# Kernel tuning notes

Hardware: AMD Instinct MI355X
Metric: run time of the kernel (lower is better)

Reference implementation:

```python
import jax, jax.numpy as jnp
import numpy as np

N = 8192
H = 512
E = 262144
NUM_LAYERS = 2
LAYER_DECAY = 0.4
INIT_W = 1e-05


def setup_inputs() -> dict:
    key = jax.random.key(0)
    ks = jax.random.split(key, 6)
    x = jax.random.normal(ks[0], (N, H), dtype=jnp.float32)
    rows = jax.random.randint(ks[1], (E,), 0, N, dtype=jnp.int32)
    cols = jax.random.randint(ks[2], (E,), 0, N, dtype=jnp.int32)
    vals = jax.random.uniform(ks[3], (E,), dtype=jnp.float32)
    # near-identity init as in GSS_GNNLayer (torch Linear: y = x @ W.T + b)
    W1 = jax.random.normal(ks[4], (H, H), dtype=jnp.float32) * INIT_W + jnp.eye(H, dtype=jnp.float32)
    b1 = jnp.zeros((H,), dtype=jnp.float32)
    W2 = jax.random.normal(ks[5], (H, H), dtype=jnp.float32) * INIT_W + jnp.eye(H, dtype=jnp.float32)
    b2 = jnp.zeros((H,), dtype=jnp.float32)
    return {"x": x, "rows": rows, "cols": cols, "vals": vals,
            "W1": W1, "b1": b1, "W2": W2, "b2": b2}


def _spmm(rows, cols, vals, dense):
    # sparse [N,N] @ dense [N,H] via gather + segment-sum scatter-add
    return jax.ops.segment_sum(vals[:, None] * dense[cols], rows, num_segments=N)


def _gcn_layer(x, rows, cols, vals, W1, b1, W2, b2):
    Ax = _spmm(rows, cols, vals, x)                      # [N,H]
    pre1 = Ax @ W1.T + b1
    Ax_x = _spmm(rows, cols, vals, Ax * x)               # A(Ax * x)
    pre2 = Ax_x @ W2.T + b2
    pre = pre1 + pre2
    return pre, jax.nn.elu(pre)


def reference(x, rows, cols, vals, W1, b1, W2, b2):
    residual = None
    for _ in range(NUM_LAYERS):  # shared weights across layers, as in source
        pre, x = _gcn_layer(x, rows, cols, vals, W1, b1, W2, b2)
        if residual is not None:
            x = residual + LAYER_DECAY * x
        residual = pre
    # decoder: row-wise L2 normalize (eps=1e-12 like F.normalize), dense gram, relu
    norm = jnp.maximum(jnp.linalg.norm(x, axis=1, keepdims=True), 1e-12)
    hidden_emb = x / norm
    adj_preds = jax.nn.relu(hidden_emb @ hidden_emb.T)   # [N,N]
    return adj_preds, hidden_emb
```

## Files before the change

### kernel.cpp

```cpp
#include <hip/hip_runtime.h>

#define N_NODES 8192
#define HDIM    512
#define NEDGE   262144

typedef __attribute__((ext_vector_type(8))) short bf16x8;
typedef __attribute__((ext_vector_type(4))) short bf16x4;
typedef __attribute__((ext_vector_type(4))) float f32x4;

__device__ inline unsigned short f2bf(float f) {
  unsigned u = __float_as_uint(f);
  unsigned r = (u + 0x7FFFu + ((u >> 16) & 1u)) >> 16;
  return (unsigned short)r;
}
__device__ inline float bf2f(short s) {
  return __uint_as_float(((unsigned)(unsigned short)s) << 16);
}

__device__ inline void gload16(const void* g, void* l) {
  __builtin_amdgcn_global_load_lds(
      (const __attribute__((address_space(1))) unsigned*)g,
      (__attribute__((address_space(3))) unsigned*)l, 16, 0, 0);
}

__global__ void hist_kernel(const int* __restrict__ rows, int* __restrict__ counts) {
  int e = blockIdx.x * 256 + threadIdx.x;
  atomicAdd(&counts[rows[e]], 1);
}

__global__ __launch_bounds__(1024) void scan_kernel(const int* __restrict__ counts,
                                                    int* __restrict__ offs,
                                                    int* __restrict__ cursor) {
  __shared__ int s[1024];
  int tid = threadIdx.x;
  int local[8];
  int sum = 0;
#pragma unroll
  for (int i = 0; i < 8; ++i) { local[i] = counts[tid * 8 + i]; sum += local[i]; }
  s[tid] = sum;
  __syncthreads();
  for (int d = 1; d < 1024; d <<= 1) {
    int v = (tid >= d) ? s[tid - d] : 0;
    __syncthreads();
    s[tid] += v;
    __syncthreads();
  }
  int base = (tid > 0) ? s[tid - 1] : 0;
#pragma unroll
  for (int i = 0; i < 8; ++i) {
    offs[tid * 8 + i] = base;
    cursor[tid * 8 + i] = base;
    base += local[i];
  }
  if (tid == 1023) offs[8192] = base;
}

__global__ void scatter_kernel(const int* __restrict__ rows, const int* __restrict__ cols,
                               const float* __restrict__ vals, int* cursor,
                               int2* __restrict__ edges) {
  int e = blockIdx.x * 256 + threadIdx.x;
  int slot = atomicAdd(&cursor[rows[e]], 1);
  edges[slot] = make_int2(cols[e], __float_as_int(vals[e]));
}

template <int MODE>
__global__ __launch_bounds__(256) void spmm_bf(const int* __restrict__ offs,
                                               const int2* __restrict__ edges,
                                               const short* __restrict__ Xbf,
                                               const float* __restrict__ aux,
                                               short* __restrict__ outb,
                                               short* __restrict__ prodb) {
  int row = blockIdx.x * 4 + (threadIdx.x >> 6);
  int lane = threadIdx.x & 63;
  int h0 = lane * 8;
  float acc[8] = {0.f, 0.f, 0.f, 0.f, 0.f, 0.f, 0.f, 0.f};
  int e0 = offs[row], e1 = offs[row + 1];
  int p = e0;

  int2 ma0, ma1, ma2, ma3;
  bf16x8 xa0, xa1, xa2, xa3;

  if (p + 4 <= e1) {
    ma0 = edges[p]; ma1 = edges[p + 1]; ma2 = edges[p + 2]; ma3 = edges[p + 3];
    xa0 = *reinterpret_cast<const bf16x8*>(Xbf + (size_t)ma0.x * HDIM + h0);
    xa1 = *reinterpret_cast<const bf16x8*>(Xbf + (size_t)ma1.x * HDIM + h0);
    xa2 = *reinterpret_cast<const bf16x8*>(Xbf + (size_t)ma2.x * HDIM + h0);
    xa3 = *reinterpret_cast<const bf16x8*>(Xbf + (size_t)ma3.x * HDIM + h0);
    p += 4;
    for (; p + 4 <= e1; p += 4) {
      int2 mb0 = edges[p], mb1 = edges[p + 1], mb2 = edges[p + 2], mb3 = edges[p + 3];
      bf16x8 xb0 = *reinterpret_cast<const bf16x8*>(Xbf + (size_t)mb0.x * HDIM + h0);
      bf16x8 xb1 = *reinterpret_cast<const bf16x8*>(Xbf + (size_t)mb1.x * HDIM + h0);
      bf16x8 xb2 = *reinterpret_cast<const bf16x8*>(Xbf + (size_t)mb2.x * HDIM + h0);
      bf16x8 xb3 = *reinterpret_cast<const bf16x8*>(Xbf + (size_t)mb3.x * HDIM + h0);
      float v0 = __int_as_float(ma0.y), v1 = __int_as_float(ma1.y);
      float v2 = __int_as_float(ma2.y), v3 = __int_as_float(ma3.y);
#pragma unroll
      for (int j = 0; j < 8; ++j) {
        acc[j] = fmaf(v0, bf2f(xa0[j]), acc[j]);
        acc[j] = fmaf(v1, bf2f(xa1[j]), acc[j]);
        acc[j] = fmaf(v2, bf2f(xa2[j]), acc[j]);
        acc[j] = fmaf(v3, bf2f(xa3[j]), acc[j]);
      }
      ma0 = mb0; ma1 = mb1; ma2 = mb2; ma3 = mb3;
      xa0 = xb0; xa1 = xb1; xa2 = xb2; xa3 = xb3;
    }
    {
      float v0 = __int_as_float(ma0.y), v1 = __int_as_float(ma1.y);
      float v2 = __int_as_float(ma2.y), v3 = __int_as_float(ma3.y);
#pragma unroll
      for (int j = 0; j < 8; ++j) {
        acc[j] = fmaf(v0, bf2f(xa0[j]), acc[j]);
        acc[j] = fmaf(v1, bf2f(xa1[j]), acc[j]);
        acc[j] = fmaf(v2, bf2f(xa2[j]), acc[j]);
        acc[j] = fmaf(v3, bf2f(xa3[j]), acc[j]);
      }
    }
  }
  for (; p < e1; ++p) {
    int2 e = edges[p];
    float v = __int_as_float(e.y);
    bf16x8 xr = *reinterpret_cast<const bf16x8*>(Xbf + (size_t)e.x * HDIM + h0);
#pragma unroll
    for (int j = 0; j < 8; ++j) acc[j] = fmaf(v, bf2f(xr[j]), acc[j]);
  }

  bf16x8 o;
#pragma unroll
  for (int j = 0; j < 8; ++j) o[j] = (short)f2bf(acc[j]);
  *reinterpret_cast<bf16x8*>(outb + (size_t)row * 1024 + h0) = o;
  if (MODE != 2) {
    const float4* ap = reinterpret_cast<const float4*>(aux + (size_t)row * HDIM + h0);
    float4 a0 = ap[0], a1 = ap[1];
    float xv[8] = {a0.x, a0.y, a0.z, a0.w, a1.x, a1.y, a1.z, a1.w};
    if (MODE == 1) {
#pragma unroll
      for (int j = 0; j < 8; ++j) xv[j] = xv[j] > 0.f ? xv[j] : expm1f(xv[j]);
    }
    bf16x8 t;
#pragma unroll
    for (int j = 0; j < 8; ++j) t[j] = (short)f2bf(acc[j] * xv[j]);
    *reinterpret_cast<bf16x8*>(prodb + (size_t)row * HDIM + h0) = t;
  }
}

__device__ inline void cast8(const float* src, short* dst) {
  const float4* p = reinterpret_cast<const float4*>(src);
  float4 a = p[0], b = p[1];
  bf16x8 o;
  o[0] = (short)f2bf(a.x); o[1] = (short)f2bf(a.y);
  o[2] = (short)f2bf(a.z); o[3] = (short)f2bf(a.w);
  o[4] = (short)f2bf(b.x); o[5] = (short)f2bf(b.y);
  o[6] = (short)f2bf(b.z); o[7] = (short)f2bf(b.w);
  *reinterpret_cast<bf16x8*>(dst) = o;
}

__global__ void prep_kernel(const float* __restrict__ x,
                            const float* __restrict__ W1, const float* __restrict__ W2,
                            const float* __restrict__ b1, const float* __restrict__ b2,
                            short* __restrict__ Xbf, short* __restrict__ Bbuf,
                            float* __restrict__ b12) {
  int b = blockIdx.x;
  if (b < 2048) {
    int t = b * 256 + threadIdx.x;
    int row = t >> 6, c0 = (t & 63) * 8;
    cast8(x + (size_t)row * 512 + c0, Xbf + (size_t)row * 512 + c0);
  } else if (b < 2176) {
    int t = (b - 2048) * 256 + threadIdx.x;
    int row = t >> 6, c0 = (t & 63) * 8;
    cast8(W1 + (size_t)row * 512 + c0, Bbuf + (size_t)row * 1024 + c0);
  } else if (b < 2304) {
    int t = (b - 2176) * 256 + threadIdx.x;
    int row = t >> 6, c0 = (t & 63) * 8;
    cast8(W2 + (size_t)row * 512 + c0, Bbuf + (size_t)row * 1024 + 512 + c0);
  } else {
    int j = threadIdx.x;
    b12[j] = b1[j] + b2[j];
    b12[j + 256] = b1[j + 256] + b2[j + 256];
  }
}

__global__ __launch_bounds__(256) void rownorm_kernel(const float* __restrict__ X,
                                                      float* __restrict__ outf,
                                                      short* __restrict__ outb) {
  int row = blockIdx.x * 4 + (threadIdx.x >> 6);
  int lane = threadIdx.x & 63;
  int h0 = lane * 8;
  const float4* p = reinterpret_cast<const float4*>(X + (size_t)row * HDIM + h0);
  float4 a = p[0], b = p[1];
  float s = a.x * a.x + a.y * a.y + a.z * a.z + a.w * a.w +
            b.x * b.x + b.y * b.y + b.z * b.z + b.w * b.w;
#pragma unroll
  for (int off = 1; off < 64; off <<= 1) s += __shfl_xor(s, off, 64);
  float inv = 1.f / fmaxf(sqrtf(s), 1e-12f);
  a.x *= inv; a.y *= inv; a.z *= inv; a.w *= inv;
  b.x *= inv; b.y *= inv; b.z *= inv; b.w *= inv;
  float4* q = reinterpret_cast<float4*>(outf + (size_t)row * HDIM + h0);
  q[0] = a; q[1] = b;
  bf16x8 o;
  o[0] = (short)f2bf(a.x); o[1] = (short)f2bf(a.y);
  o[2] = (short)f2bf(a.z); o[3] = (short)f2bf(a.w);
  o[4] = (short)f2bf(b.x); o[5] = (short)f2bf(b.y);
  o[6] = (short)f2bf(b.z); o[7] = (short)f2bf(b.w);
  *reinterpret_cast<bf16x8*>(outb + (size_t)row * HDIM + h0) = o;
}

template <int MODE>
__global__ __launch_bounds__(256) void gemm_lds(const short* __restrict__ A,
                                                const short* __restrict__ B,
                                                int N, int K, int nbn,
                                                const float* __restrict__ bias,
                                                const float* __restrict__ resid,
                                                float* __restrict__ out0,
                                                short* __restrict__ out1bf) {
  __shared__ __align__(16) short la[128 * 64];
  __shared__ __align__(16) short lb[128 * 64];

  int q = gridDim.x >> 3;
  int id = (blockIdx.x & 7) * q + (blockIdx.x >> 3);
  int bn = (id % nbn) * 128;
  int bm = (id / nbn) * 128;

  int lane = threadIdx.x & 63;
  int wave = threadIdx.x >> 6;

  int rsub = lane >> 3;
  int csrc = (lane & 7) ^ rsub;
  size_t ldkB = (size_t)K * 2;
  const char* gA0 = (const char*)A + (size_t)(bm + wave * 32 + rsub) * ldkB + csrc * 16;
  const char* gB0 = (const char*)B + (size_t)(bn + wave * 32 + rsub) * ldkB + csrc * 16;
  char* lA0 = (char*)la + wave * 4096;
  char* lB0 = (char*)lb + wave * 4096;

  f32x4 zero = {0.f, 0.f, 0.f, 0.f};
  f32x4 acc[4][4];
#pragma unroll
  for (int m = 0; m < 4; ++m)
#pragma unroll
    for (int n = 0; n < 4; ++n) acc[m][n] = zero;

  int rlo = lane & 15;
  int khi = lane >> 4;
  int wm = wave >> 1, wn = wave & 1;

  for (int k0 = 0; k0 < K; k0 += 64) {
    __syncthreads();
#pragma unroll
    for (int j = 0; j < 4; ++j) {
      gload16(gA0 + (size_t)j * 8 * ldkB + (size_t)k0 * 2, lA0 + j * 1024);
      gload16(gB0 + (size_t)j * 8 * ldkB + (size_t)k0 * 2, lB0 + j * 1024);
    }
    __syncthreads();
#pragma unroll
    for (int kk = 0; kk < 2; ++kk) {
      bf16x8 av[4], bv[4];
#pragma unroll
      for (int m = 0; m < 4; ++m) {
        int ra = wm * 64 + m * 16 + rlo;
        int pc = (kk * 4 + khi) ^ (ra & 7);
        av[m] = *reinterpret_cast<const bf16x8*>((const char*)la + ra * 128 + pc * 16);
      }
#pragma unroll
      for (int n = 0; n < 4; ++n) {
        int rb = wn * 64 + n * 16 + rlo;
        int pc = (kk * 4 + khi) ^ (rb & 7);
        bv[n] = *reinterpret_cast<const bf16x8*>((const char*)lb + rb * 128 + pc * 16);
      }
#pragma unroll
      for (int m = 0; m < 4; ++m)
#pragma unroll
        for (int n = 0; n < 4; ++n)
          acc[m][n] = __builtin_amdgcn_mfma_f32_16x16x32_bf16(av[m], bv[n], acc[m][n], 0, 0, 0);
    }
  }

  int obm = bm + wm * 64;
  int obn = bn + wn * 64;
  int crow = (lane >> 4) * 4;
  int ccol = lane & 15;
#pragma unroll
  for (int n = 0; n < 4; ++n) {
    int c = obn + n * 16 + ccol;
    float bc = bias[c];
#pragma unroll
    for (int m = 0; m < 4; ++m) {
#pragma unroll
      for (int v = 0; v < 4; ++v) {
        int r = obm + m * 16 + crow + v;
        size_t idx = (size_t)r * N + c;
        float val = acc[m][n][v];
        if (MODE == 0) {
          float pvl = val + bc;
          out0[idx] = pvl;
          float e = pvl > 0.f ? pvl : expm1f(pvl);
          out1bf[idx] = (short)f2bf(e);
        } else {
          float pvl = val + bc;
          out0[idx] = resid[idx] + 0.4f * (pvl > 0.f ? pvl : expm1f(pvl));
        }
      }
    }
  }
}

__global__ __launch_bounds__(512, 4) void gram256(const short* __restrict__ H,
                                                  float* __restrict__ out) {
  __shared__ __align__(16) char lds[3 * 24576];
  const int NK = HDIM / 32;

  int id = (blockIdx.x & 7) * 256 + (blockIdx.x >> 3);
  int st = id >> 4, wt = id & 15;
  int bm = ((st >> 3) * 4 + (wt >> 2)) * 128;
  int bn = ((st & 7) * 4 + (wt & 3)) * 256;

  int tid = threadIdx.x;
  int wid = tid >> 6;
  int lane = tid & 63;
  int wr = wid >> 2;
  int wc = wid & 3;
  int rlo = lane & 15;
  int khi = lane >> 4;
  int wbase = wid * 1024;

  const char* Ab = (const char*)H + (size_t)bm * 1024;
  const char* Bb = (const char*)H + (size_t)bn * 1024;
  int r4 = tid >> 2, c4 = tid & 3;

  f32x4 zero = {0.f, 0.f, 0.f, 0.f};
  f32x4 acc[4][4];
#pragma unroll
  for (int m = 0; m < 4; ++m)
#pragma unroll
    for (int n = 0; n < 4; ++n) acc[m][n] = zero;

  auto stage = [&](int s) {
    char* slot = lds + (s % 3) * 24576;
    size_t go = (size_t)s * 64 + c4 * 16;
    gload16(Ab + (size_t)r4 * 1024 + go,         slot + wbase);
    gload16(Bb + (size_t)r4 * 1024 + go,         slot + 8192 + wbase);
    gload16(Bb + (size_t)(r4 + 128) * 1024 + go, slot + 16384 + wbase);
  };

  stage(0);

  for (int s = 0; s < NK; ++s) {
    if (s + 1 < NK) {
      stage(s + 1);
      asm volatile("s_waitcnt vmcnt(3)" ::: "memory");
    } else {
      asm volatile("s_waitcnt vmcnt(0)" ::: "memory");
    }
    __builtin_amdgcn_s_barrier();
    __builtin_amdgcn_sched_barrier(0);

    const char* slot = lds + (s % 3) * 24576;
    bf16x8 av[4], bv[4];
#pragma unroll
    for (int m = 0; m < 4; ++m)
      av[m] = *reinterpret_cast<const bf16x8*>(
          slot + (wr * 64 + m * 16 + rlo) * 64 + khi * 16);
#pragma unroll
    for (int n = 0; n < 4; ++n)
      bv[n] = *reinterpret_cast<const bf16x8*>(
          slot + 8192 + (wc * 64 + n * 16 + rlo) * 64 + khi * 16);

    __builtin_amdgcn_s_setprio(1);
#pragma unroll
    for (int m = 0; m < 4; ++m)
#pragma unroll
      for (int n = 0; n < 4; ++n)
        acc[m][n] = __builtin_amdgcn_mfma_f32_16x16x32_bf16(av[m], bv[n], acc[m][n], 0, 0, 0);
    __builtin_amdgcn_s_setprio(0);
  }

  int obm = bm + wr * 64;
  int obn = bn + wc * 64;
  int crow = khi * 4;
#pragma unroll
  for (int m = 0; m < 4; ++m) {
#pragma unroll
    for (int n = 0; n < 4; ++n) {
      int c = obn + n * 16 + rlo;
#pragma unroll
      for (int v = 0; v < 4; ++v) {
        int r = obm + m * 16 + crow + v;
        float val = acc[m][n][v];
        out[(size_t)r * N_NODES + c] = val > 0.f ? val : 0.f;
      }
    }
  }
}

extern "C" void kernel_launch(void* const* d_in, const int* in_sizes, int n_in,
                              void* d_out, int out_size, void* d_ws, size_t ws_size,
                              hipStream_t stream) {
  const float* x  = (const float*)d_in[0];
  const int* rows = (const int*)d_in[1];
  const int* cols = (const int*)d_in[2];
  const float* vals = (const float*)d_in[3];
  const float* W1 = (const float*)d_in[4];
  const float* b1 = (const float*)d_in[5];
  const float* W2 = (const float*)d_in[6];
  const float* b2 = (const float*)d_in[7];

  float* out_adj = (float*)d_out;
  float* out_hid = out_adj + (size_t)N_NODES * N_NODES;

  char* w = (char*)d_ws;
  size_t off = 0;
  auto alloc = [&](size_t bytes) -> void* {
    void* p = w + off;
    off += (bytes + 255) & ~(size_t)255;
    return p;
  };
  int* counts   = (int*)alloc(8192 * sizeof(int));
  int* offs     = (int*)alloc(8193 * sizeof(int));
  int* cursor   = (int*)alloc(8192 * sizeof(int));
  int2* edges   = (int2*)alloc((size_t)NEDGE * sizeof(int2));
  float* b12    = (float*)alloc(HDIM * sizeof(float));
  short* Xbf    = (short*)alloc((size_t)N_NODES * HDIM * sizeof(short));
  short* Tbf    = (short*)alloc((size_t)N_NODES * HDIM * sizeof(short));
  short* Abuf   = (short*)alloc((size_t)N_NODES * 1024 * sizeof(short));
  short* Bbuf   = (short*)alloc((size_t)512 * 1024 * sizeof(short));
  float* pre1   = (float*)alloc((size_t)N_NODES * HDIM * sizeof(float));
  float* Hf     = (float*)alloc((size_t)N_NODES * HDIM * sizeof(float));
  short* Hbuf   = (short*)alloc((size_t)N_NODES * HDIM * sizeof(short));

  hipMemsetAsync(counts, 0, 8192 * sizeof(int), stream);
  hist_kernel<<<NEDGE / 256, 256, 0, stream>>>(rows, counts);
  scan_kernel<<<1, 1024, 0, stream>>>(counts, offs, cursor);
  scatter_kernel<<<NEDGE / 256, 256, 0, stream>>>(rows, cols, vals, cursor, edges);

  prep_kernel<<<2305, 256, 0, stream>>>(x, W1, W2, b1, b2, Xbf, Bbuf, b12);

  spmm_bf<0><<<2048, 256, 0, stream>>>(offs, edges, Xbf, x, Abuf, Tbf);
  spmm_bf<2><<<2048, 256, 0, stream>>>(offs, edges, Tbf, nullptr, Abuf + 512, nullptr);
  gemm_lds<0><<<256, 256, 0, stream>>>(Abuf, Bbuf, 512, 1024, 4, b12, nullptr, pre1, Xbf);

  spmm_bf<1><<<2048, 256, 0, stream>>>(offs, edges, Xbf, pre1, Abuf, Tbf);
  spmm_bf<2><<<2048, 256, 0, stream>>>(offs, edges, Tbf, nullptr, Abuf + 512, nullptr);
  gemm_lds<1><<<256, 256, 0, stream>>>(Abuf, Bbuf, 512, 1024, 4, b12, pre1, Hf, nullptr);

  rownorm_kernel<<<2048, 256, 0, stream>>>(Hf, out_hid, Hbuf);
  gram256<<<2048, 512, 0, stream>>>(Hbuf, out_adj);
}
```

Baseline: 327.3 us.

## Add triple-buffered async LDS ring to dense GEMM, fuse histogram into prep

Replaces the GEMM's synchronous load-then-compute K loop (two barriers per 64-wide step) with a three-slot LDS ring. Two K=32 stages are prefetched ahead, paced by vmcnt waits and a single barrier per step. The gram kernel's prefetch moves from one stage ahead to two, with the next load issued after the barrier. The edge histogram is folded into the prep kernel to remove one launch. These changes aim to hide global-load latency and cut launch overhead, at the cost of dropping the XOR-swizzled LDS layout, which may bring bank conflicts.

After: 315.7 us. 1.04x faster.

```diff
diff --git a/kernel.cpp b/kernel.cpp
--- a/kernel.cpp
+++ b/kernel.cpp
@@ -5,7 +5,6 @@
 #define NEDGE   262144
 
 typedef __attribute__((ext_vector_type(8))) short bf16x8;
-typedef __attribute__((ext_vector_type(4))) short bf16x4;
 typedef __attribute__((ext_vector_type(4))) float f32x4;
 
 __device__ inline unsigned short f2bf(float f) {
@@ -23,9 +22,11 @@
       (__attribute__((address_space(3))) unsigned*)l, 16, 0, 0);
 }
 
-__global__ void hist_kernel(const int* __restrict__ rows, int* __restrict__ counts) {
-  int e = blockIdx.x * 256 + threadIdx.x;
-  atomicAdd(&counts[rows[e]], 1);
+__device__ inline void wait_vmcnt_c(int n) {
+  if (n == 8)      asm volatile("s_waitcnt vmcnt(8)" ::: "memory");
+  else if (n == 4) asm volatile("s_waitcnt vmcnt(4)" ::: "memory");
+  else if (n == 3) asm volatile("s_waitcnt vmcnt(3)" ::: "memory");
+  else             asm volatile("s_waitcnt vmcnt(0)" ::: "memory");
 }
 
 __global__ __launch_bounds__(1024) void scan_kernel(const int* __restrict__ counts,
@@ -155,22 +156,26 @@
   *reinterpret_cast<bf16x8*>(dst) = o;
 }
 
-__global__ void prep_kernel(const float* __restrict__ x,
+__global__ void prep_kernel(const int* __restrict__ rows, int* __restrict__ counts,
+                            const float* __restrict__ x,
                             const float* __restrict__ W1, const float* __restrict__ W2,
                             const float* __restrict__ b1, const float* __restrict__ b2,
                             short* __restrict__ Xbf, short* __restrict__ Bbuf,
                             float* __restrict__ b12) {
   int b = blockIdx.x;
-  if (b < 2048) {
-    int t = b * 256 + threadIdx.x;
+  if (b < 1024) {
+    int e = b * 256 + threadIdx.x;
+    atomicAdd(&counts[rows[e]], 1);
+  } else if (b < 3072) {
+    int t = (b - 1024) * 256 + threadIdx.x;
     int row = t >> 6, c0 = (t & 63) * 8;
     cast8(x + (size_t)row * 512 + c0, Xbf + (size_t)row * 512 + c0);
-  } else if (b < 2176) {
-    int t = (b - 2048) * 256 + threadIdx.x;
+  } else if (b < 3200) {
+    int t = (b - 3072) * 256 + threadIdx.x;
     int row = t >> 6, c0 = (t & 63) * 8;
     cast8(W1 + (size_t)row * 512 + c0, Bbuf + (size_t)row * 1024 + c0);
-  } else if (b < 2304) {
-    int t = (b - 2176) * 256 + threadIdx.x;
+  } else if (b < 3328) {
+    int t = (b - 3200) * 256 + threadIdx.x;
     int row = t >> 6, c0 = (t & 63) * 8;
     cast8(W2 + (size_t)row * 512 + c0, Bbuf + (size_t)row * 1024 + 512 + c0);
   } else {
@@ -206,31 +211,33 @@
 }
 
 template <int MODE>
-__global__ __launch_bounds__(256) void gemm_lds(const short* __restrict__ A,
-                                                const short* __restrict__ B,
-                                                int N, int K, int nbn,
-                                                const float* __restrict__ bias,
-                                                const float* __restrict__ resid,
-                                                float* __restrict__ out0,
-                                                short* __restrict__ out1bf) {
-  __shared__ __align__(16) short la[128 * 64];
-  __shared__ __align__(16) short lb[128 * 64];
+__global__ __launch_bounds__(256) void gemm_ring(const short* __restrict__ A,
+                                                 const short* __restrict__ B,
+                                                 int N, int K, int nbn,
+                                                 const float* __restrict__ bias,
+                                                 const float* __restrict__ resid,
+                                                 float* __restrict__ out0,
+                                                 short* __restrict__ out1bf) {
+  __shared__ __align__(16) char lds[3 * 16384];
+  int NK = K >> 5;
 
   int q = gridDim.x >> 3;
   int id = (blockIdx.x & 7) * q + (blockIdx.x >> 3);
   int bn = (id % nbn) * 128;
   int bm = (id / nbn) * 128;
 
-  int lane = threadIdx.x & 63;
-  int wave = threadIdx.x >> 6;
-
-  int rsub = lane >> 3;
-  int csrc = (lane & 7) ^ rsub;
+  int tid = threadIdx.x;
+  int wid = tid >> 6;
+  int lane = tid & 63;
+  int wm = wid >> 1, wn = wid & 1;
+  int rlo = lane & 15;
+  int khi = lane >> 4;
+  int wbase = wid * 1024;
+
   size_t ldkB = (size_t)K * 2;
-  const char* gA0 = (const char*)A + (size_t)(bm + wave * 32 + rsub) * ldkB + csrc * 16;
-  const char* gB0 = (const char*)B + (size_t)(bn + wave * 32 + rsub) * ldkB + csrc * 16;
-  char* lA0 = (char*)la + wave * 4096;
-  char* lB0 = (char*)lb + wave * 4096;
+  const char* Ab = (const char*)A + (size_t)bm * ldkB;
+  const char* Bb = (const char*)B + (size_t)bn * ldkB;
+  int r4 = tid >> 2, c4 = tid & 3;
 
   f32x4 zero = {0.f, 0.f, 0.f, 0.f};
   f32x4 acc[4][4];
@@ -239,48 +246,50 @@
 #pragma unroll
     for (int n = 0; n < 4; ++n) acc[m][n] = zero;
 
-  int rlo = lane & 15;
-  int khi = lane >> 4;
-  int wm = wave >> 1, wn = wave & 1;
-
-  for (int k0 = 0; k0 < K; k0 += 64) {
-    __syncthreads();
-#pragma unroll
-    for (int j = 0; j < 4; ++j) {
-      gload16(gA0 + (size_t)j * 8 * ldkB + (size_t)k0 * 2, lA0 + j * 1024);
-      gload16(gB0 + (size_t)j * 8 * ldkB + (size_t)k0 * 2, lB0 + j * 1024);
-    }
-    __syncthreads();
-#pragma unroll
-    for (int kk = 0; kk < 2; ++kk) {
-      bf16x8 av[4], bv[4];
-#pragma unroll
-      for (int m = 0; m < 4; ++m) {
-        int ra = wm * 64 + m * 16 + rlo;
-        int pc = (kk * 4 + khi) ^ (ra & 7);
-        av[m] = *reinterpret_cast<const bf16x8*>((const char*)la + ra * 128 + pc * 16);
-      }
-#pragma unroll
-      for (int n = 0; n < 4; ++n) {
-        int rb = wn * 64 + n * 16 + rlo;
-        int pc = (kk * 4 + khi) ^ (rb & 7);
-        bv[n] = *reinterpret_cast<const bf16x8*>((const char*)lb + rb * 128 + pc * 16);
-      }
-#pragma unroll
-      for (int m = 0; m < 4; ++m)
-#pragma unroll
-        for (int n = 0; n < 4; ++n)
-          acc[m][n] = __builtin_amdgcn_mfma_f32_16x16x32_bf16(av[m], bv[n], acc[m][n], 0, 0, 0);
-    }
+  auto stage = [&](int s) {
+    char* slot = lds + (s % 3) * 16384;
+    size_t go = (size_t)s * 64 + c4 * 16;
+    gload16(Ab + (size_t)r4 * ldkB + go,         slot + wbase);
+    gload16(Ab + (size_t)(r4 + 64) * ldkB + go,  slot + 4096 + wbase);
+    gload16(Bb + (size_t)r4 * ldkB + go,         slot + 8192 + wbase);
+    gload16(Bb + (size_t)(r4 + 64) * ldkB + go,  slot + 12288 + wbase);
+  };
+
+  stage(0);
+  stage(1);
+
+  for (int s = 0; s < NK; ++s) {
+    wait_vmcnt_c((s + 1 < NK) ? 4 : 0);
+    __builtin_amdgcn_s_barrier();
+    __builtin_amdgcn_sched_barrier(0);
+    if (s + 2 < NK) stage(s + 2);
+
+    const char* slot = lds + (s % 3) * 16384;
+    bf16x8 av[4], bv[4];
+#pragma unroll
+    for (int m = 0; m < 4; ++m)
+      av[m] = *reinterpret_cast<const bf16x8*>(
+          slot + (wm * 64 + m * 16 + rlo) * 64 + khi * 16);
+#pragma unroll
+    for (int n = 0; n < 4; ++n)
+      bv[n] = *reinterpret_cast<const bf16x8*>(
+          slot + 8192 + (wn * 64 + n * 16 + rlo) * 64 + khi * 16);
+
+    __builtin_amdgcn_s_setprio(1);
+#pragma unroll
+    for (int m = 0; m < 4; ++m)
+#pragma unroll
+      for (int n = 0; n < 4; ++n)
+        acc[m][n] = __builtin_amdgcn_mfma_f32_16x16x32_bf16(av[m], bv[n], acc[m][n], 0, 0, 0);
+    __builtin_amdgcn_s_setprio(0);
   }
 
   int obm = bm + wm * 64;
   int obn = bn + wn * 64;
-  int crow = (lane >> 4) * 4;
-  int ccol = lane & 15;
+  int crow = khi * 4;
 #pragma unroll
   for (int n = 0; n < 4; ++n) {
-    int c = obn + n * 16 + ccol;
+    int c = obn + n * 16 + rlo;
     float bc = bias[c];
 #pragma unroll
     for (int m = 0; m < 4; ++m) {
@@ -342,16 +351,13 @@
   };
 
   stage(0);
+  stage(1);
 
   for (int s = 0; s < NK; ++s) {
-    if (s + 1 < NK) {
-      stage(s + 1);
-      asm volatile("s_waitcnt vmcnt(3)" ::: "memory");
-    } else {
-      asm volatile("s_waitcnt vmcnt(0)" ::: "memory");
-    }
+    wait_vmcnt_c((s + 1 < NK) ? 3 : 0);
     __builtin_amdgcn_s_barrier();
     __builtin_amdgcn_sched_barrier(0);
+    if (s + 2 < NK) stage(s + 2);
 
     const char* slot = lds + (s % 3) * 24576;
     bf16x8 av[4], bv[4];
@@ -427,19 +433,17 @@
   short* Hbuf   = (short*)alloc((size_t)N_NODES * HDIM * sizeof(short));
 
   hipMemsetAsync(counts, 0, 8192 * sizeof(int), stream);
-  hist_kernel<<<NEDGE / 256, 256, 0, stream>>>(rows, counts);
+  prep_kernel<<<3329, 256, 0, stream>>>(rows, counts, x, W1, W2, b1, b2, Xbf, Bbuf, b12);
   scan_kernel<<<1, 1024, 0, stream>>>(counts, offs, cursor);
   scatter_kernel<<<NEDGE / 256, 256, 0, stream>>>(rows, cols, vals, cursor, edges);
 
-  prep_kernel<<<2305, 256, 0, stream>>>(x, W1, W2, b1, b2, Xbf, Bbuf, b12);
-
   spmm_bf<0><<<2048, 256, 0, stream>>>(offs, edges, Xbf, x, Abuf, Tbf);
   spmm_bf<2><<<2048, 256, 0, stream>>>(offs, edges, Tbf, nullptr, Abuf + 512, nullptr);
-  gemm_lds<0><<<256, 256, 0, stream>>>(Abuf, Bbuf, 512, 1024, 4, b12, nullptr, pre1, Xbf);
+  gemm_ring<0><<<256, 256, 0, stream>>>(Abuf, Bbuf, 512, 1024, 4, b12, nullptr, pre1, Xbf);
 
   spmm_bf<1><<<2048, 256, 0, stream>>>(offs, edges, Xbf, pre1, Abuf, Tbf);
   spmm_bf<2><<<2048, 256, 0, stream>>>(offs, edges, Tbf, nullptr, Abuf + 512, nullptr);
-  gemm_lds<1><<<256, 256, 0, stream>>>(Abuf, Bbuf, 512, 1024, 4, b12, pre1, Hf, nullptr);
+  gemm_ring<1><<<256, 256, 0, stream>>>(Abuf, Bbuf, 512, 1024, 4, b12, pre1, Hf, nullptr);
 
   rownorm_kernel<<<2048, 256, 0, stream>>>(Hf, out_hid, Hbuf);
   gram256<<<2048, 512, 0, stream>>>(Hbuf, out_adj);
```
